# Optimization experiments

Hardware: AMD Instinct MI355X
Metric: run time of the kernel (lower is better)

## Reference

```python
import jax, jax.numpy as jnp
import numpy as np

H = 1024      # LSTM_DIM
D = 1024      # BERT_DIM
VW = 30000    # word vocab
VA = 30       # action vocab
T = 64        # transition steps
S = 512       # BERT memory length


def lstm_cell(x, h, c, Wih, Whh, bih, bhh):
    # torch.nn.LSTMCell math: gates ordered i, f, g, o
    g = x @ Wih.T + bih + h @ Whh.T + bhh
    i, f, gg, o = jnp.split(g, 4, axis=-1)
    c2 = jax.nn.sigmoid(f) * c + jax.nn.sigmoid(i) * jnp.tanh(gg)
    h2 = jax.nn.sigmoid(o) * jnp.tanh(c2)
    return h2, c2


def forward(memory, actions, words,
            term_Wih, term_Whh, term_bih, term_bhh,
            act_Wih, act_Whh, act_bih, act_bhh,
            Wq, bq, Wa1, ba1, Wa2, ba2, Ww1, bw1, Ww2, bw2,
            act_emb, word_emb):
    z = jnp.zeros((1, H), dtype=memory.dtype)

    def step(carry, xs):
        term_h, term_c, act_h, act_c, stack_h = carry
        a_t, w_t = xs
        # predict_action: concat decoder states, dot-attention over BERT memory (no softmax)
        states = jnp.concatenate([term_h, act_h, stack_h], axis=1)     # [1, 3H]
        q = states @ Wq.T + bq                                          # [1, D]
        attn = jnp.einsum('bsd,bd->bs', memory, q)                      # [1, S]
        ctx = jnp.einsum('bs,bsd->bd', attn, memory)                    # [1, D]
        final = jnp.concatenate([states, ctx], axis=1)                  # [1, 3H+D]
        act_logits = jax.nn.relu(final @ Wa1.T + ba1) @ Wa2.T + ba2     # [1, VA]
        word_logits = jax.nn.relu(final @ Ww1.T + bw1) @ Ww2.T + bw2    # [1, VW]
        # do_action: act LSTM step, then SHIFT: word embedding into term LSTM + stack push
        a_e = act_emb[a_t][None, :]
        act_h2, act_c2 = lstm_cell(a_e, act_h, act_c, act_Wih, act_Whh, act_bih, act_bhh)
        w_e = word_emb[w_t][None, :]
        term_h2, term_c2 = lstm_cell(w_e, term_h, term_c, term_Wih, term_Whh, term_bih, term_bhh)
        new_carry = (term_h2, term_c2, act_h2, act_c2, w_e)
        return new_carry, (act_logits[0], word_logits[0])

    carry0 = (z, z, z, z, z)
    _, (act_logits, word_logits) = jax.lax.scan(step, carry0, (actions, words))
    return act_logits, word_logits  # [T, VA], [T, VW]


def setup_inputs() -> dict:
    key = jax.random.key(0)
    ks = jax.random.split(key, 24)
    s = 0.02

    def n(k, shape):
        return jax.random.normal(k, shape, dtype=jnp.float32) * s

    return {
        'memory': jax.random.normal(ks[0], (1, S, D), dtype=jnp.float32),
        'actions': jax.random.randint(ks[1], (T,), 0, VA),
        'words': jax.random.randint(ks[2], (T,), 0, VW),
        'term_Wih': n(ks[3], (4 * H, H)), 'term_Whh': n(ks[4], (4 * H, H)),
        'term_bih': n(ks[5], (4 * H,)), 'term_bhh': n(ks[6], (4 * H,)),
        'act_Wih': n(ks[7], (4 * H, H)), 'act_Whh': n(ks[8], (4 * H, H)),
        'act_bih': n(ks[9], (4 * H,)), 'act_bhh': n(ks[10], (4 * H,)),
        'Wq': n(ks[11], (D, 3 * H)), 'bq': n(ks[12], (D,)),
        'Wa1': n(ks[13], (H, 3 * H + D)), 'ba1': n(ks[14], (H,)),
        'Wa2': n(ks[15], (VA, H)), 'ba2': n(ks[16], (VA,)),
        'Ww1': n(ks[17], (H, 3 * H + D)), 'bw1': n(ks[18], (H,)),
        'Ww2': n(ks[19], (VW, H)), 'bw2': n(ks[20], (VW,)),
        'act_emb': n(ks[21], (VA, H)),
        'word_emb': n(ks[22], (VW, H)),
    }


def reference(memory, actions, words,
              term_Wih, term_Whh, term_bih, term_bhh,
              act_Wih, act_Whh, act_bih, act_bhh,
              Wq, bq, Wa1, ba1, Wa2, ba2, Ww1, bw1, Ww2, bw2,
              act_emb, word_emb):
    return forward(memory, actions, words,
                   term_Wih, term_Whh, term_bih, term_bhh,
                   act_Wih, act_Whh, act_bih, act_bhh,
                   Wq, bq, Wa1, ba1, Wa2, ba2, Ww1, bw1, Ww2, bw2,
                   act_emb, word_emb)
```

## Files before the change

kernel.cpp:

```cpp
#include <hip/hip_runtime.h>

#define H 1024
#define T_STEPS 64
#define S_MEM 512
#define VA 30
#define VW 30000

typedef unsigned long long u64;

__device__ __forceinline__ float sigmf(float x) { return 1.f / (1.f + expf(-x)); }

__global__ __launch_bounds__(256) void k_init(
    const int* __restrict__ actions, const int* __restrict__ words,
    const float* __restrict__ act_emb, const float* __restrict__ word_emb,
    float* __restrict__ X_term, float* __restrict__ X_act,
    float* __restrict__ fin, u64* __restrict__ htag) {
  int b = blockIdx.x, tid = threadIdx.x;
  if (b < T_STEPS) {
    int wi = words[b], ai = actions[b];
    for (int i = tid; i < H; i += 256) {
      float we = word_emb[(size_t)wi * H + i];
      X_term[b * H + i] = we;
      X_act[b * H + i]  = act_emb[(size_t)ai * H + i];
      if (b + 1 < T_STEPS) fin[(size_t)(b + 1) * 4096 + 2048 + i] = we;
    }
    if (b == 0)
      for (int i = tid; i < H; i += 256) fin[2048 + i] = 0.f;
  } else if (b == T_STEPS) {
    for (int i = tid; i < H; i += 256) { fin[i] = 0.f; fin[H + i] = 0.f; }
  } else {
    for (int i = (b - 65) * 256 + tid; i < 64 * 2048; i += 64 * 256) htag[i] = 0ull;
  }
}

template<bool BT>
__global__ __launch_bounds__(256) void k_gemm64(
    const float* __restrict__ A, int lda,
    const float* __restrict__ B, int ldb,
    int N, int K,
    float* __restrict__ Ppart,
    const float* __restrict__ bias, const float* __restrict__ bias2, int relu,
    float* __restrict__ Cfinal, int ldc) {
  __shared__ __align__(16) float As[64 * 64];
  __shared__ __align__(16) float Bs[64 * 64];
  const float4* As4 = (const float4*)As;
  const float4* Bs4 = (const float4*)Bs;
  int tid = threadIdx.x;
  int cidx = tid & 15;
  int ridx = tid >> 4;
  int n0 = blockIdx.x * 64;
  int splitk = gridDim.y;
  int klen = K / splitk;
  int kbeg = blockIdx.y * klen;
  float acc[4][4] = {};

  for (int k0 = kbeg; k0 < kbeg + klen; k0 += 64) {
#pragma unroll
    for (int i = 0; i < 4; ++i) {
      int f = tid + i * 256;
      int rr = f >> 4, km = f & 15;
      float4 v = *(const float4*)&A[(size_t)rr * lda + k0 + km * 4];
      int c2 = ((rr >> 2) ^ km) & 15, p = rr & 3;
      As[(km * 4 + 0) * 64 + c2 * 4 + p] = v.x;
      As[(km * 4 + 1) * 64 + c2 * 4 + p] = v.y;
      As[(km * 4 + 2) * 64 + c2 * 4 + p] = v.z;
      As[(km * 4 + 3) * 64 + c2 * 4 + p] = v.w;
    }
    if (BT) {
#pragma unroll
      for (int i = 0; i < 4; ++i) {
        int f = tid + i * 256;
        int nn = f >> 4, km = f & 15;
        int gn = n0 + nn;
        float4 v = make_float4(0.f, 0.f, 0.f, 0.f);
        if (gn < N) v = *(const float4*)&B[(size_t)gn * ldb + k0 + km * 4];
        int c2 = ((nn >> 2) ^ km) & 15, p = nn & 3;
        Bs[(km * 4 + 0) * 64 + c2 * 4 + p] = v.x;
        Bs[(km * 4 + 1) * 64 + c2 * 4 + p] = v.y;
        Bs[(km * 4 + 2) * 64 + c2 * 4 + p] = v.z;
        Bs[(km * 4 + 3) * 64 + c2 * 4 + p] = v.w;
      }
    } else {
#pragma unroll
      for (int i = 0; i < 4; ++i) {
        int f = tid + i * 256;
        int kr = f >> 4, nq = f & 15;
        int gn = n0 + nq * 4;
        float4 v = make_float4(0.f, 0.f, 0.f, 0.f);
        if (gn < N) v = *(const float4*)&B[(size_t)(k0 + kr) * ldb + gn];
        ((float4*)Bs)[kr * 16 + ((nq ^ (kr >> 2)) & 15)] = v;
      }
    }
    __syncthreads();
#pragma unroll 8
    for (int kk = 0; kk < 64; ++kk) {
      int sw = kk >> 2;
      float4 a4 = As4[kk * 16 + ((ridx ^ sw) & 15)];
      float4 b4 = Bs4[kk * 16 + ((cidx ^ sw) & 15)];
      float av[4] = {a4.x, a4.y, a4.z, a4.w};
      float bv[4] = {b4.x, b4.y, b4.z, b4.w};
#pragma unroll
      for (int i = 0; i < 4; ++i)
#pragma unroll
        for (int j = 0; j < 4; ++j) acc[i][j] += av[i] * bv[j];
    }
    __syncthreads();
  }

  int gcol = n0 + cidx * 4;
  if (splitk > 1) {
    float* P = Ppart + (size_t)blockIdx.y * 64 * N;
    if (gcol < N) {
#pragma unroll
      for (int i = 0; i < 4; ++i) {
        int row = ridx * 4 + i;
        *(float4*)&P[(size_t)row * N + gcol] =
            make_float4(acc[i][0], acc[i][1], acc[i][2], acc[i][3]);
      }
    }
  } else {
    if (gcol < N) {
      float4 bs = bias ? *(const float4*)&bias[gcol] : make_float4(0, 0, 0, 0);
      if (bias2) {
        float4 b2 = *(const float4*)&bias2[gcol];
        bs.x += b2.x; bs.y += b2.y; bs.z += b2.z; bs.w += b2.w;
      }
#pragma unroll
      for (int i = 0; i < 4; ++i) {
        int row = ridx * 4 + i;
        float4 v = make_float4(acc[i][0] + bs.x, acc[i][1] + bs.y,
                               acc[i][2] + bs.z, acc[i][3] + bs.w);
        if (relu) {
          v.x = fmaxf(v.x, 0.f); v.y = fmaxf(v.y, 0.f);
          v.z = fmaxf(v.z, 0.f); v.w = fmaxf(v.w, 0.f);
        }
        *(float4*)&Cfinal[(size_t)row * ldc + gcol] = v;
      }
    }
  }
}

__global__ __launch_bounds__(256) void k_gemm_dual(
    const float* __restrict__ A0, const float* __restrict__ A1, int lda,
    const float* __restrict__ B0, const float* __restrict__ B1, int ldb,
    int N, int K, float* __restrict__ P0, float* __restrict__ P1) {
  __shared__ __align__(16) float As[64 * 64];
  __shared__ __align__(16) float Bs[64 * 64];
  const float4* As4 = (const float4*)As;
  const float4* Bs4 = (const float4*)Bs;
  const float* A = blockIdx.z ? A1 : A0;
  const float* B = blockIdx.z ? B1 : B0;
  float* Pp = blockIdx.z ? P1 : P0;
  int tid = threadIdx.x;
  int cidx = tid & 15;
  int ridx = tid >> 4;
  int n0 = blockIdx.x * 64;
  int klen = K / gridDim.y;
  int kbeg = blockIdx.y * klen;
  float acc[4][4] = {};

  for (int k0 = kbeg; k0 < kbeg + klen; k0 += 64) {
#pragma unroll
    for (int i = 0; i < 4; ++i) {
      int f = tid + i * 256;
      int rr = f >> 4, km = f & 15;
      float4 v = *(const float4*)&A[(size_t)rr * lda + k0 + km * 4];
      int c2 = ((rr >> 2) ^ km) & 15, p = rr & 3;
      As[(km * 4 + 0) * 64 + c2 * 4 + p] = v.x;
      As[(km * 4 + 1) * 64 + c2 * 4 + p] = v.y;
      As[(km * 4 + 2) * 64 + c2 * 4 + p] = v.z;
      As[(km * 4 + 3) * 64 + c2 * 4 + p] = v.w;
    }
#pragma unroll
    for (int i = 0; i < 4; ++i) {
      int f = tid + i * 256;
      int nn = f >> 4, km = f & 15;
      int gn = n0 + nn;
      float4 v = make_float4(0.f, 0.f, 0.f, 0.f);
      if (gn < N) v = *(const float4*)&B[(size_t)gn * ldb + k0 + km * 4];
      int c2 = ((nn >> 2) ^ km) & 15, p = nn & 3;
      Bs[(km * 4 + 0) * 64 + c2 * 4 + p] = v.x;
      Bs[(km * 4 + 1) * 64 + c2 * 4 + p] = v.y;
      Bs[(km * 4 + 2) * 64 + c2 * 4 + p] = v.z;
      Bs[(km * 4 + 3) * 64 + c2 * 4 + p] = v.w;
    }
    __syncthreads();
#pragma unroll 8
    for (int kk = 0; kk < 64; ++kk) {
      int sw = kk >> 2;
      float4 a4 = As4[kk * 16 + ((ridx ^ sw) & 15)];
      float4 b4 = Bs4[kk * 16 + ((cidx ^ sw) & 15)];
      float av[4] = {a4.x, a4.y, a4.z, a4.w};
      float bv[4] = {b4.x, b4.y, b4.z, b4.w};
#pragma unroll
      for (int i = 0; i < 4; ++i)
#pragma unroll
        for (int j = 0; j < 4; ++j) acc[i][j] += av[i] * bv[j];
    }
    __syncthreads();
  }
  int gcol = n0 + cidx * 4;
  float* P = Pp + (size_t)blockIdx.y * 64 * N;
  if (gcol < N) {
#pragma unroll
    for (int i = 0; i < 4; ++i) {
      int row = ridx * 4 + i;
      *(float4*)&P[(size_t)row * N + gcol] =
          make_float4(acc[i][0], acc[i][1], acc[i][2], acc[i][3]);
    }
  }
}

__global__ __launch_bounds__(256) void k_reduce4(
    const float* __restrict__ P, int S, int N,
    const float* __restrict__ bias, const float* __restrict__ bias2, int relu,
    float* __restrict__ out, int ldc) {
  int q = blockIdx.x * 256 + threadIdx.x;
  int total = 64 * N / 4;
  if (q >= total) return;
  int e0 = q * 4;
  int row = e0 / N, col = e0 - row * N;
  float4 v = make_float4(0, 0, 0, 0);
  for (int s = 0; s < S; ++s) {
    float4 p = *(const float4*)&P[(size_t)s * 64 * N + e0];
    v.x += p.x; v.y += p.y; v.z += p.z; v.w += p.w;
  }
  if (bias) {
    float4 b = *(const float4*)&bias[col];
    v.x += b.x; v.y += b.y; v.z += b.z; v.w += b.w;
  }
  if (bias2) {
    float4 b = *(const float4*)&bias2[col];
    v.x += b.x; v.y += b.y; v.z += b.z; v.w += b.w;
  }
  if (relu) {
    v.x = fmaxf(v.x, 0.f); v.y = fmaxf(v.y, 0.f);
    v.z = fmaxf(v.z, 0.f); v.w = fmaxf(v.w, 0.f);
  }
  *(float4*)&out[(size_t)row * ldc + col] = v;
}

__global__ __launch_bounds__(256) void k_reduce_dual(
    const float* __restrict__ P0, const float* __restrict__ P1, int S, int N,
    const float* __restrict__ ba0, const float* __restrict__ ba1,
    const float* __restrict__ bb0, const float* __restrict__ bb1,
    float* __restrict__ o0, float* __restrict__ o1, int relu) {
  const float* P = blockIdx.y ? P1 : P0;
  const float* bias = blockIdx.y ? ba1 : ba0;
  const float* bias2 = blockIdx.y ? bb1 : bb0;
  float* out = blockIdx.y ? o1 : o0;
  int q = blockIdx.x * 256 + threadIdx.x;
  int total = 64 * N / 4;
  if (q >= total) return;
  int e0 = q * 4;
  int col = e0 % N;
  float4 v = make_float4(0, 0, 0, 0);
  for (int s = 0; s < S; ++s) {
    float4 p = *(const float4*)&P[(size_t)s * 64 * N + e0];
    v.x += p.x; v.y += p.y; v.z += p.z; v.w += p.w;
  }
  if (bias) {
    float4 b = *(const float4*)&bias[col];
    v.x += b.x; v.y += b.y; v.z += b.z; v.w += b.w;
  }
  if (bias2) {
    float4 b = *(const float4*)&bias2[col];
    v.x += b.x; v.y += b.y; v.z += b.z; v.w += b.w;
  }
  if (relu) {
    v.x = fmaxf(v.x, 0.f); v.y = fmaxf(v.y, 0.f);
    v.z = fmaxf(v.z, 0.f); v.w = fmaxf(v.w, 0.f);
  }
  *(float4*)&out[e0] = v;
}

__global__ __launch_bounds__(512, 1) void k_recur(
    const float* __restrict__ Whh_term, const float* __restrict__ Whh_act,
    const float* __restrict__ xg_term, const float* __restrict__ xg_act,
    float* __restrict__ fin, u64* __restrict__ htag) {
  __shared__ __align__(16) float wlds[32 * 1024];
  __shared__ __align__(16) float hs[2][1024];
  __shared__ float xgs[63 * 32];
  int b = blockIdx.x, tid = threadIdx.x;
  int lstm = b >> 7, k0 = (b & 127) * 8;
  const float* Whh = lstm ? Whh_act : Whh_term;
  const float* xg  = lstm ? xg_act : xg_term;
  int d = tid >> 6, p = tid & 63;

  for (int f = tid; f < 8192; f += 512) {
    int r = f >> 8, q = f & 255;
    int g = r >> 3, dd = r & 7;
    float4 v = *(const float4*)&Whh[(size_t)((g << 10) + k0 + dd) * 1024 + q * 4];
    *(float4*)&wlds[r * 1024 + q * 4] = v;
  }
  for (int i = tid; i < 63 * 32; i += 512) {
    int rr = i & 31;
    xgs[i] = xg[(size_t)(i >> 5) * 4096 + (size_t)(rr >> 3) * 1024 + k0 + (rr & 7)];
  }
  __syncthreads();

  float c_loc = 0.f;

  for (int t = 0; t < 63; ++t) {
    float* hb = hs[t & 1];
    if (t > 0) {
      const u64* src = htag + (size_t)t * 2048 + lstm * 1024;
      u64 v0 = __hip_atomic_load(&src[tid], __ATOMIC_RELAXED, __HIP_MEMORY_SCOPE_AGENT);
      u64 v1 = __hip_atomic_load(&src[tid + 512], __ATOMIC_RELAXED, __HIP_MEMORY_SCOPE_AGENT);
      while ((unsigned)(v0 >> 32) != (unsigned)t)
        v0 = __hip_atomic_load(&src[tid], __ATOMIC_RELAXED, __HIP_MEMORY_SCOPE_AGENT);
      while ((unsigned)(v1 >> 32) != (unsigned)t)
        v1 = __hip_atomic_load(&src[tid + 512], __ATOMIC_RELAXED, __HIP_MEMORY_SCOPE_AGENT);
      hb[tid]       = __uint_as_float((unsigned)v0);
      hb[tid + 512] = __uint_as_float((unsigned)v1);
    } else {
      hb[tid] = 0.f;
      hb[tid + 512] = 0.f;
    }
    __syncthreads();

    float s0 = 0.f, s1 = 0.f, s2 = 0.f, s3 = 0.f;
#pragma unroll
    for (int s = 0; s < 4; ++s) {
      int off = s * 256 + p * 4;
      float4 hv = *(const float4*)&hb[off];
      float4 w0 = *(const float4*)&wlds[(d << 10) + off];
      float4 w1 = *(const float4*)&wlds[((8 + d) << 10) + off];
      float4 w2 = *(const float4*)&wlds[((16 + d) << 10) + off];
      float4 w3 = *(const float4*)&wlds[((24 + d) << 10) + off];
      s0 += w0.x * hv.x + w0.y * hv.y + w0.z * hv.z + w0.w * hv.w;
      s1 += w1.x * hv.x + w1.y * hv.y + w1.z * hv.z + w1.w * hv.w;
      s2 += w2.x * hv.x + w2.y * hv.y + w2.z * hv.z + w2.w * hv.w;
      s3 += w3.x * hv.x + w3.y * hv.y + w3.z * hv.z + w3.w * hv.w;
    }
#pragma unroll
    for (int m = 1; m <= 32; m <<= 1) {
      s0 += __shfl_xor(s0, m); s1 += __shfl_xor(s1, m);
      s2 += __shfl_xor(s2, m); s3 += __shfl_xor(s3, m);
    }
    if (p == 0) {
      float gi = s0 + xgs[t * 32 + d];
      float gf = s1 + xgs[t * 32 + 8 + d];
      float gg = s2 + xgs[t * 32 + 16 + d];
      float go = s3 + xgs[t * 32 + 24 + d];
      float c2 = sigmf(gf) * c_loc + sigmf(gi) * tanhf(gg);
      float h2 = sigmf(go) * tanhf(c2);
      c_loc = c2;
      fin[(size_t)(t + 1) * 4096 + lstm * 1024 + k0 + d] = h2;
      __hip_atomic_store(&htag[(size_t)(t + 1) * 2048 + lstm * 1024 + k0 + d],
                         (((u64)(t + 1)) << 32) | (u64)__float_as_uint(h2),
                         __ATOMIC_RELAXED, __HIP_MEMORY_SCOPE_AGENT);
    }
  }
}

__global__ __launch_bounds__(256) void k_actlog(
    const float* __restrict__ ha, const float* __restrict__ Wa2,
    const float* __restrict__ ba2, float* __restrict__ out) {
  int t = blockIdx.x, tid = threadIdx.x;
  int v = tid >> 3, p = tid & 7;
  float sum = 0.f;
  if (v < VA) {
    const float* a  = ha + (size_t)t * 1024 + p * 128;
    const float* wr = Wa2 + (size_t)v * 1024 + p * 128;
#pragma unroll 8
    for (int i = 0; i < 128; i += 4) {
      float4 av = *(const float4*)(a + i);
      float4 wv = *(const float4*)(wr + i);
      sum += av.x * wv.x + av.y * wv.y + av.z * wv.z + av.w * wv.w;
    }
  }
  sum += __shfl_xor(sum, 1);
  sum += __shfl_xor(sum, 2);
  sum += __shfl_xor(sum, 4);
  if (p == 0 && v < VA) out[(size_t)t * VA + v] = sum + ba2[v];
}

extern "C" void kernel_launch(void* const* d_in, const int* in_sizes, int n_in,
                              void* d_out, int out_size, void* d_ws, size_t ws_size,
                              hipStream_t stream) {
  const float* memory   = (const float*)d_in[0];
  const int*   actions  = (const int*)d_in[1];
  const int*   words    = (const int*)d_in[2];
  const float* term_Wih = (const float*)d_in[3];
  const float* term_Whh = (const float*)d_in[4];
  const float* term_bih = (const float*)d_in[5];
  const float* term_bhh = (const float*)d_in[6];
  const float* act_Wih  = (const float*)d_in[7];
  const float* act_Whh  = (const float*)d_in[8];
  const float* act_bih  = (const float*)d_in[9];
  const float* act_bhh  = (const float*)d_in[10];
  const float* Wq  = (const float*)d_in[11];
  const float* bq  = (const float*)d_in[12];
  const float* Wa1 = (const float*)d_in[13];
  const float* ba1 = (const float*)d_in[14];
  const float* Wa2 = (const float*)d_in[15];
  const float* ba2 = (const float*)d_in[16];
  const float* Ww1 = (const float*)d_in[17];
  const float* bw1 = (const float*)d_in[18];
  const float* Ww2 = (const float*)d_in[19];
  const float* bw2 = (const float*)d_in[20];
  const float* act_emb  = (const float*)d_in[21];
  const float* word_emb = (const float*)d_in[22];
  float* out = (float*)d_out;

  float* w       = (float*)d_ws;
  float* X_term  = w;
  float* X_act   = X_term + 65536;
  float* xg_term = X_act + 65536;
  float* xg_act  = xg_term + 262144;
  float* fin     = xg_act + 262144;
  float* qbuf    = fin + 262144;
  float* attn    = qbuf + 65536;
  float* ha      = attn + 32768;
  float* hw      = ha + 65536;
  u64*   htag    = (u64*)(hw + 65536);
  float* P       = (float*)(htag + 64 * 2048);

  size_t base_fl = (size_t)(P - w);
  int wsplit = (ws_size >= (base_fl + 2ull * 64 * VW + 1024) * 4) ? 2 : 1;

  k_init<<<129, 256, 0, stream>>>(actions, words, act_emb, word_emb,
                                  X_term, X_act, fin, htag);

  k_gemm_dual<<<dim3(64, 2, 2), 256, 0, stream>>>(
      X_term, X_act, 1024, term_Wih, act_Wih, 1024, 4096, 1024, P, P + 524288);
  k_reduce_dual<<<dim3(256, 2), 256, 0, stream>>>(
      P, P + 524288, 2, 4096, term_bih, act_bih, term_bhh, act_bhh, xg_term, xg_act, 0);

  k_recur<<<256, 512, 0, stream>>>(term_Whh, act_Whh, xg_term, xg_act, fin, htag);

  k_gemm64<true><<<dim3(16, 8), 256, 0, stream>>>(fin, 4096, Wq, 3072, 1024, 3072,
                                                  P, nullptr, nullptr, 0, nullptr, 0);
  k_reduce4<<<64, 256, 0, stream>>>(P, 8, 1024, bq, nullptr, 0, qbuf, 1024);

  k_gemm64<true><<<dim3(8, 8), 256, 0, stream>>>(qbuf, 1024, memory, 1024, 512, 1024,
                                                 P, nullptr, nullptr, 0, nullptr, 0);
  k_reduce4<<<32, 256, 0, stream>>>(P, 8, 512, nullptr, nullptr, 0, attn, 512);

  k_gemm64<false><<<dim3(16, 8), 256, 0, stream>>>(attn, 512, memory, 1024, 1024, 512,
                                                   P, nullptr, nullptr, 0, nullptr, 0);
  k_reduce4<<<64, 256, 0, stream>>>(P, 8, 1024, nullptr, nullptr, 0, fin + 3072, 4096);

  k_gemm_dual<<<dim3(16, 8, 2), 256, 0, stream>>>(
      fin, fin, 4096, Wa1, Ww1, 4096, 1024, 4096, P, P + 524288);
  k_reduce_dual<<<dim3(64, 2), 256, 0, stream>>>(
      P, P + 524288, 8, 1024, ba1, bw1, nullptr, nullptr, ha, hw, 1);

  k_actlog<<<64, 256, 0, stream>>>(ha, Wa2, ba2, out);

  if (wsplit == 2) {
    k_gemm64<true><<<dim3(469, 2), 256, 0, stream>>>(hw, 1024, Ww2, 1024, VW, 1024,
                                                     P, nullptr, nullptr, 0, nullptr, 0);
    k_reduce4<<<1875, 256, 0, stream>>>(P, 2, VW, bw2, nullptr, 0, out + 1920, VW);
  } else {
    k_gemm64<true><<<dim3(469, 1), 256, 0, stream>>>(hw, 1024, Ww2, 1024, VW, 1024,
                                                     nullptr, bw2, nullptr, 0, out + 1920, VW);
  }
}
```

Baseline: 533.4 us.

## Replace per-step block barrier with single-wave poll and LDS flag handoff

```diff
diff --git a/kernel.cpp b/kernel.cpp
--- a/kernel.cpp
+++ b/kernel.cpp
@@ -281,11 +281,12 @@
   __shared__ __align__(16) float wlds[32 * 1024];
   __shared__ __align__(16) float hs[2][1024];
   __shared__ float xgs[63 * 32];
+  __shared__ int flag;
   int b = blockIdx.x, tid = threadIdx.x;
   int lstm = b >> 7, k0 = (b & 127) * 8;
   const float* Whh = lstm ? Whh_act : Whh_term;
   const float* xg  = lstm ? xg_act : xg_term;
-  int d = tid >> 6, p = tid & 63;
+  int w = tid >> 6, p = tid & 63;
 
   for (int f = tid; f < 8192; f += 512) {
     int r = f >> 8, q = f & 255;
@@ -297,59 +298,81 @@
     int rr = i & 31;
     xgs[i] = xg[(size_t)(i >> 5) * 4096 + (size_t)(rr >> 3) * 1024 + k0 + (rr & 7)];
   }
+  if (tid == 0) flag = 0;
   __syncthreads();
 
   float c_loc = 0.f;
 
   for (int t = 0; t < 63; ++t) {
-    float* hb = hs[t & 1];
     if (t > 0) {
-      const u64* src = htag + (size_t)t * 2048 + lstm * 1024;
-      u64 v0 = __hip_atomic_load(&src[tid], __ATOMIC_RELAXED, __HIP_MEMORY_SCOPE_AGENT);
-      u64 v1 = __hip_atomic_load(&src[tid + 512], __ATOMIC_RELAXED, __HIP_MEMORY_SCOPE_AGENT);
-      while ((unsigned)(v0 >> 32) != (unsigned)t)
-        v0 = __hip_atomic_load(&src[tid], __ATOMIC_RELAXED, __HIP_MEMORY_SCOPE_AGENT);
-      while ((unsigned)(v1 >> 32) != (unsigned)t)
-        v1 = __hip_atomic_load(&src[tid + 512], __ATOMIC_RELAXED, __HIP_MEMORY_SCOPE_AGENT);
-      hb[tid]       = __uint_as_float((unsigned)v0);
-      hb[tid + 512] = __uint_as_float((unsigned)v1);
-    } else {
-      hb[tid] = 0.f;
-      hb[tid + 512] = 0.f;
-    }
-    __syncthreads();
+      if (w == 0) {
+        const u64* src = htag + (size_t)t * 2048 + lstm * 1024 + p * 16;
+        u64 v[16];
+#pragma unroll
+        for (int j = 0; j < 16; ++j)
+          v[j] = __hip_atomic_load(&src[j], __ATOMIC_RELAXED, __HIP_MEMORY_SCOPE_AGENT);
+        bool ok;
+        do {
+          ok = true;
+#pragma unroll
+          for (int j = 0; j < 16; ++j) {
+            if ((unsigned)(v[j] >> 32) != (unsigned)t) {
+              v[j] = __hip_atomic_load(&src[j], __ATOMIC_RELAXED, __HIP_MEMORY_SCOPE_AGENT);
+              ok = false;
+            }
+          }
+        } while (!ok);
+        float* hb = hs[t & 1];
+#pragma unroll
+        for (int q = 0; q < 4; ++q) {
+          float4 f4;
+          f4.x = __uint_as_float((unsigned)v[q * 4 + 0]);
+          f4.y = __uint_as_float((unsigned)v[q * 4 + 1]);
+          f4.z = __uint_as_float((unsigned)v[q * 4 + 2]);
+          f4.w = __uint_as_float((unsigned)v[q * 4 + 3]);
+          *(float4*)&hb[p * 16 + q * 4] = f4;
+        }
+        if (p == 0)
+          __hip_atomic_store(&flag, t, __ATOMIC_RELEASE, __HIP_MEMORY_SCOPE_WORKGROUP);
+      } else {
+        while (__hip_atomic_load(&flag, __ATOMIC_ACQUIRE, __HIP_MEMORY_SCOPE_WORKGROUP) < t) {}
+      }
+    }
 
     float s0 = 0.f, s1 = 0.f, s2 = 0.f, s3 = 0.f;
-#pragma unroll
-    for (int s = 0; s < 4; ++s) {
-      int off = s * 256 + p * 4;
-      float4 hv = *(const float4*)&hb[off];
-      float4 w0 = *(const float4*)&wlds[(d << 10) + off];
-      float4 w1 = *(const float4*)&wlds[((8 + d) << 10) + off];
-      float4 w2 = *(const float4*)&wlds[((16 + d) << 10) + off];
-      float4 w3 = *(const float4*)&wlds[((24 + d) << 10) + off];
-      s0 += w0.x * hv.x + w0.y * hv.y + w0.z * hv.z + w0.w * hv.w;
-      s1 += w1.x * hv.x + w1.y * hv.y + w1.z * hv.z + w1.w * hv.w;
-      s2 += w2.x * hv.x + w2.y * hv.y + w2.z * hv.z + w2.w * hv.w;
-      s3 += w3.x * hv.x + w3.y * hv.y + w3.z * hv.z + w3.w * hv.w;
-    }
-#pragma unroll
-    for (int m = 1; m <= 32; m <<= 1) {
-      s0 += __shfl_xor(s0, m); s1 += __shfl_xor(s1, m);
-      s2 += __shfl_xor(s2, m); s3 += __shfl_xor(s3, m);
+    if (t > 0) {
+      const float* hb = hs[t & 1];
+#pragma unroll
+      for (int s = 0; s < 4; ++s) {
+        int off = s * 256 + p * 4;
+        float4 hv = *(const float4*)&hb[off];
+        float4 w0 = *(const float4*)&wlds[(w << 10) + off];
+        float4 w1 = *(const float4*)&wlds[((8 + w) << 10) + off];
+        float4 w2 = *(const float4*)&wlds[((16 + w) << 10) + off];
+        float4 w3 = *(const float4*)&wlds[((24 + w) << 10) + off];
+        s0 += w0.x * hv.x + w0.y * hv.y + w0.z * hv.z + w0.w * hv.w;
+        s1 += w1.x * hv.x + w1.y * hv.y + w1.z * hv.z + w1.w * hv.w;
+        s2 += w2.x * hv.x + w2.y * hv.y + w2.z * hv.z + w2.w * hv.w;
+        s3 += w3.x * hv.x + w3.y * hv.y + w3.z * hv.z + w3.w * hv.w;
+      }
+#pragma unroll
+      for (int m = 1; m <= 32; m <<= 1) {
+        s0 += __shfl_xor(s0, m); s1 += __shfl_xor(s1, m);
+        s2 += __shfl_xor(s2, m); s3 += __shfl_xor(s3, m);
+      }
     }
     if (p == 0) {
-      float gi = s0 + xgs[t * 32 + d];
-      float gf = s1 + xgs[t * 32 + 8 + d];
-      float gg = s2 + xgs[t * 32 + 16 + d];
-      float go = s3 + xgs[t * 32 + 24 + d];
+      float gi = s0 + xgs[t * 32 + w];
+      float gf = s1 + xgs[t * 32 + 8 + w];
+      float gg = s2 + xgs[t * 32 + 16 + w];
+      float go = s3 + xgs[t * 32 + 24 + w];
       float c2 = sigmf(gf) * c_loc + sigmf(gi) * tanhf(gg);
       float h2 = sigmf(go) * tanhf(c2);
       c_loc = c2;
-      fin[(size_t)(t + 1) * 4096 + lstm * 1024 + k0 + d] = h2;
-      __hip_atomic_store(&htag[(size_t)(t + 1) * 2048 + lstm * 1024 + k0 + d],
+      __hip_atomic_store(&htag[(size_t)(t + 1) * 2048 + lstm * 1024 + k0 + w],
                          (((u64)(t + 1)) << 32) | (u64)__float_as_uint(h2),
                          __ATOMIC_RELAXED, __HIP_MEMORY_SCOPE_AGENT);
+      fin[(size_t)(t + 1) * 4096 + lstm * 1024 + k0 + w] = h2;
     }
   }
 }
```

After: 961.3 us. 1.8x slower.
